# Optimization experiments

Hardware: AMD Instinct MI355X
Metric: run time of the kernel (lower is better)

The kernel has to match this reference:

```python
import jax, jax.numpy as jnp
import numpy as np

N = 100000   # nodes
E = 1600000  # edges (avg degree 16)
IN, HID, OUT = 128, 128, 64


def _glorot(key, shape):
    limit = np.sqrt(6.0 / (shape[0] + shape[1])).astype(np.float32)
    return jax.random.uniform(key, shape, jnp.float32, -limit, limit)


def setup_inputs() -> dict:
    key = jax.random.key(0)
    ks = jax.random.split(key, 12)
    inp = {}
    for i, (f, s, d) in enumerate([("feat1", "src1", "dst1"), ("feat2", "src2", "dst2"), ("feat", "src", "dst")]):
        inp[f] = jax.random.normal(ks[3 * i], (N, IN), jnp.float32)
        inp[s] = jax.random.randint(ks[3 * i + 1], (E,), 0, N, jnp.int32)
        inp[d] = jax.random.randint(ks[3 * i + 2], (E,), 0, N, jnp.int32)
    inp["W1"] = _glorot(ks[9], (IN, HID))
    inp["b1"] = jnp.zeros((HID,), jnp.float32)
    inp["W2"] = _glorot(ks[10], (HID, OUT))
    inp["b2"] = jnp.zeros((OUT,), jnp.float32)
    return inp


def _gcn_layer(x, src, dst, W, b):
    # DGL GraphConv norm='both': D_dst^{-1/2} * A * D_src^{-1/2} * X * W + b
    ones = jnp.ones(src.shape, jnp.float32)
    deg_out = jax.ops.segment_sum(ones, src, num_segments=N)
    deg_in = jax.ops.segment_sum(ones, dst, num_segments=N)
    norm_src = jax.lax.rsqrt(jnp.maximum(deg_out, 1.0))
    norm_dst = jax.lax.rsqrt(jnp.maximum(deg_in, 1.0))
    h = (x @ W) * norm_src[:, None]           # transform then normalize (math-equivalent order)
    agg = jax.ops.segment_sum(h[src], dst, num_segments=N)  # spmm aggregate
    return agg * norm_dst[:, None] + b


def _encoder(x, src, dst, W1, b1, W2, b2):
    h = jax.nn.relu(_gcn_layer(x, src, dst, W1, b1))
    return _gcn_layer(h, src, dst, W2, b2)


def reference(feat1, src1, dst1, feat2, src2, dst2, feat, src, dst, W1, b1, W2, b2):
    z1 = _encoder(feat1, src1, dst1, W1, b1, W2, b2)
    z2 = _encoder(feat2, src2, dst2, W1, b1, W2, b2)
    z = _encoder(feat, src, dst, W1, b1, W2, b2)
    return (z1, z2, z)
```

## Files before the change

kernel.cpp:

```cpp
#include <hip/hip_runtime.h>

#define NNODES 100000
#define NEDGES 1600000
#define FIN 128
#define FHID 128
#define FOUT 64

typedef unsigned short u16;
typedef unsigned char u8;
typedef unsigned int u32;
typedef __attribute__((ext_vector_type(8))) short short8;
typedef __attribute__((ext_vector_type(4))) float floatx4;

#define NBUK 391
#define NSL2 250
#define SLICE2 (NEDGES / NSL2)
#define SP ((size_t)NSL2 * NBUK)
#define NH16 ((size_t)NNODES * FHID)

__device__ __forceinline__ u16 f2bf(float f) {
  u32 u = __float_as_uint(f);
  u32 r = (u + 0x7fffu + ((u >> 16) & 1u)) >> 16;
  return (u16)r;
}

__device__ __forceinline__ const int* sel(const int* a, const int* b, const int* c, int z) {
  return z == 0 ? a : (z == 1 ? b : c);
}


__global__ __launch_bounds__(256) void bucket_hist_kernel(
    const int* s0, const int* s1, const int* s2,
    const int* d0, const int* d1, const int* d2,
    u16* __restrict__ Hbase, int E) {
  const int z = blockIdx.z;
  const int* __restrict__ src = sel(s0, s1, s2, z);
  const int* __restrict__ dst = sel(d0, d1, d2, z);
  u32* __restrict__ part = (u32*)(Hbase + (size_t)z * NH16);
  u32* __restrict__ part_src = part + SP;
  __shared__ u32 hd[NBUK], hs[NBUK];
  const int s = blockIdx.x;
  for (int i = threadIdx.x; i < NBUK; i += 256) { hd[i] = 0; hs[i] = 0; }
  __syncthreads();
  const int e0 = s * SLICE2, e1 = min(e0 + SLICE2, E);
  const int i0 = e0 >> 2, i1 = e1 >> 2;
  for (int i = i0 + threadIdx.x; i < i1; i += 256) {
    int4 dv = ((const int4*)dst)[i];
    int4 sv = ((const int4*)src)[i];
    atomicAdd(&hd[(u32)dv.x >> 8], 1u);
    atomicAdd(&hd[(u32)dv.y >> 8], 1u);
    atomicAdd(&hd[(u32)dv.z >> 8], 1u);
    atomicAdd(&hd[(u32)dv.w >> 8], 1u);
    atomicAdd(&hs[(u32)sv.x >> 8], 1u);
    atomicAdd(&hs[(u32)sv.y >> 8], 1u);
    atomicAdd(&hs[(u32)sv.z >> 8], 1u);
    atomicAdd(&hs[(u32)sv.w >> 8], 1u);
  }
  __syncthreads();
  for (int i = threadIdx.x; i < NBUK; i += 256) {
    part[(size_t)s * NBUK + i] = hd[i];
    part_src[(size_t)s * NBUK + i] = hs[i];
  }
}

__global__ __launch_bounds__(512) void scan_part_kernel(u16* __restrict__ Hbase,
                                                        u32* __restrict__ boff_d,
                                                        u32* __restrict__ bcount_d,
                                                        u32* __restrict__ boff_s,
                                                        u32* __restrict__ bcount_s) {
  const int z = blockIdx.z;
  u32* base = (u32*)(Hbase + (size_t)z * NH16);
  u32* __restrict__ part = blockIdx.x ? base + SP : base;
  u32* __restrict__ boff = (blockIdx.x ? boff_s : boff_d) + (size_t)z * NBUK;
  u32* __restrict__ bcount = (blockIdx.x ? bcount_s : bcount_d) + (size_t)z * NBUK;
  const int b = threadIdx.x;
  u32 run = 0;
  if (b < NBUK) {
#pragma unroll 5
    for (int s = 0; s < NSL2; s++) {
      u32 v = part[(size_t)s * NBUK + b];
      part[(size_t)s * NBUK + b] = run;
      run += v;
    }
  }
  __shared__ u32 sh[512];
  sh[threadIdx.x] = (b < NBUK) ? run : 0;
  __syncthreads();
  for (int d = 1; d < 512; d <<= 1) {
    u32 t = (threadIdx.x >= d) ? sh[threadIdx.x - d] : 0;
    __syncthreads();
    sh[threadIdx.x] += t;
    __syncthreads();
  }
  if (b < NBUK) {
    boff[b] = sh[threadIdx.x] - run;
    bcount[b] = run;
  }
}

__global__ __launch_bounds__(256) void scatter_kernel(
    const int* s0, const int* s1, const int* s2,
    const int* d0, const int* d1, const int* d2,
    u16* __restrict__ Hbase, u16* __restrict__ Tbase,
    const u32* __restrict__ boff_d, const u32* __restrict__ boff_src, int E) {
  const int z = blockIdx.z;
  const int* __restrict__ src = sel(s0, s1, s2, z);
  const int* __restrict__ dst = sel(d0, d1, d2, z);
  const u32* __restrict__ part = (const u32*)(Hbase + (size_t)z * NH16);
  const u32* __restrict__ part_src = part + SP;
  u8* __restrict__ pes = (u8*)(part_src + SP);
  u32* __restrict__ pe = (u32*)(Tbase + (size_t)z * NH16);
  const u32* __restrict__ boff = boff_d + (size_t)z * NBUK;
  const u32* __restrict__ boff_s = boff_src + (size_t)z * NBUK;
  __shared__ u32 cur[NBUK], curs[NBUK];
  const int s = blockIdx.x;
  for (int i = threadIdx.x; i < NBUK; i += 256) {
    cur[i] = part[(size_t)s * NBUK + i] + boff[i];
    curs[i] = part_src[(size_t)s * NBUK + i] + boff_s[i];
  }
  __syncthreads();
  const int e0 = s * SLICE2, e1 = min(e0 + SLICE2, E);
  const int i0 = e0 >> 2, i1 = e1 >> 2;
  for (int i = i0 + threadIdx.x; i < i1; i += 256) {
    int4 sv = ((const int4*)src)[i];
    int4 dv = ((const int4*)dst)[i];
    u32 p;
    p = atomicAdd(&cur[(u32)dv.x >> 8], 1u); pe[p] = ((u32)sv.x << 8) | ((u32)dv.x & 255u);
    p = atomicAdd(&cur[(u32)dv.y >> 8], 1u); pe[p] = ((u32)sv.y << 8) | ((u32)dv.y & 255u);
    p = atomicAdd(&cur[(u32)dv.z >> 8], 1u); pe[p] = ((u32)sv.z << 8) | ((u32)dv.z & 255u);
    p = atomicAdd(&cur[(u32)dv.w >> 8], 1u); pe[p] = ((u32)sv.w << 8) | ((u32)dv.w & 255u);
    p = atomicAdd(&curs[(u32)sv.x >> 8], 1u); pes[p] = (u8)((u32)sv.x & 255u);
    p = atomicAdd(&curs[(u32)sv.y >> 8], 1u); pes[p] = (u8)((u32)sv.y & 255u);
    p = atomicAdd(&curs[(u32)sv.z >> 8], 1u); pes[p] = (u8)((u32)sv.z & 255u);
    p = atomicAdd(&curs[(u32)sv.w >> 8], 1u); pes[p] = (u8)((u32)sv.w & 255u);
  }
}

__global__ __launch_bounds__(256) void bucket_finish_kernel(
    const u16* __restrict__ Tbase, const u16* __restrict__ Hbase,
    const u32* __restrict__ boffb, const u32* __restrict__ bcountb,
    const u32* __restrict__ boff_sb, const u32* __restrict__ bcount_sb,
    int* __restrict__ csrb, int* __restrict__ offsb, int* __restrict__ degb,
    float* __restrict__ ndb, float* __restrict__ nsb, int n) {
  const int z = blockIdx.z;
  const int b = blockIdx.x;
  const int t = threadIdx.x;
  if (blockIdx.y == 1) {
    const u32* partb = (const u32*)(Hbase + (size_t)z * NH16);
    const u8* __restrict__ pes = (const u8*)(partb + 2 * SP);
    const u32* boff = boff_sb + (size_t)z * NBUK;
    const u32* bcount = bcount_sb + (size_t)z * NBUK;
    float* __restrict__ norm_src = nsb + (size_t)z * NNODES;
    const int beg = (int)boff[b];
    const int cnt = (int)bcount[b];
    __shared__ int hh[256];
    hh[t] = 0;
    __syncthreads();
    for (int i = t; i < cnt; i += 256) atomicAdd(&hh[pes[beg + i]], 1);
    __syncthreads();
    const int node = b * 256 + t;
    if (node < n) norm_src[node] = rsqrtf(fmaxf((float)hh[t], 1.0f));
    return;
  }
  const u32* __restrict__ pe = (const u32*)(Tbase + (size_t)z * NH16);
  int* __restrict__ csr = csrb + (size_t)z * NEDGES;
  int* __restrict__ offs = offsb + (size_t)z * NNODES;
  int* __restrict__ deg_dst = degb + (size_t)z * NNODES;
  float* __restrict__ norm_dst = ndb + (size_t)z * NNODES;
  const u32* boff = boffb + (size_t)z * NBUK;
  const u32* bcount = bcountb + (size_t)z * NBUK;
  const int beg = (int)boff[b];
  const int cnt = (int)bcount[b];
  __shared__ int h[256], loc[256];
  h[t] = 0;
  __syncthreads();
  for (int i = t; i < cnt; i += 256) atomicAdd(&h[pe[beg + i] & 255u], 1);
  __syncthreads();
  const int myc = h[t];
  loc[t] = myc;
  __syncthreads();
  for (int d = 1; d < 256; d <<= 1) {
    int v = (t >= d) ? loc[t - d] : 0;
    __syncthreads();
    loc[t] += v;
    __syncthreads();
  }
  const int start = beg + loc[t] - myc;
  const int node = b * 256 + t;
  if (node < n) {
    offs[node] = start;
    deg_dst[node] = myc;
    norm_dst[node] = rsqrtf(fmaxf((float)myc, 1.0f));
  }
  __syncthreads();
  h[t] = start;
  __syncthreads();
  for (int i = t; i < cnt; i += 256) {
    u32 v = pe[beg + i];
    int p = atomicAdd(&h[v & 255u], 1);
    csr[p] = (int)(v >> 8);
  }
}


#define XP 136

template <int CTOT, bool IN_BF16>
__global__ __launch_bounds__(256) void gemm_mfma(const void* X0, const void* X1,
                                                 const void* X2,
                                                 const float* __restrict__ W,
                                                 const float* __restrict__ normb,
                                                 u16* __restrict__ Yb, int nrows) {
  const int z = blockIdx.z;
  const void* __restrict__ Xv = z == 0 ? X0 : (z == 1 ? X1 : X2);
  const float* __restrict__ norm = normb + (size_t)z * NNODES;
  u16* __restrict__ Y = Yb + (size_t)z * NH16;
  __shared__ u16 Xs[64 * XP];
  __shared__ u16 Wt[64 * XP];
  __shared__ float norm_s[64];
  const int tid = threadIdx.x;
  const int row0 = blockIdx.x * 64;
  const int col0 = blockIdx.y * 64;

  if constexpr (IN_BF16) {
    const u16* X = (const u16*)Xv;
    for (int i = tid; i < 64 * 16; i += 256) {
      int r = i >> 4, k8 = (i & 15) * 8;
      int gr = row0 + r;
      uint4 v = make_uint4(0u, 0u, 0u, 0u);
      if (gr < nrows) v = *(const uint4*)&X[(size_t)gr * 128 + k8];
      *(uint4*)&Xs[r * XP + k8] = v;
    }
  } else {
    const float* X = (const float*)Xv;
    for (int i = tid; i < 64 * 32; i += 256) {
      int r = i >> 5, k4 = (i & 31) * 4;
      int gr = row0 + r;
      ushort4 o = make_ushort4(0, 0, 0, 0);
      if (gr < nrows) {
        float4 v = *(const float4*)&X[(size_t)gr * 128 + k4];
        o.x = f2bf(v.x); o.y = f2bf(v.y); o.z = f2bf(v.z); o.w = f2bf(v.w);
      }
      *(ushort4*)&Xs[r * XP + k4] = o;
    }
  }
  for (int i = tid; i < 128 * 16; i += 256) {
    int k = i >> 4, c4 = (i & 15) * 4;
    float4 v = *(const float4*)&W[(size_t)k * CTOT + col0 + c4];
    Wt[(c4 + 0) * XP + k] = f2bf(v.x);
    Wt[(c4 + 1) * XP + k] = f2bf(v.y);
    Wt[(c4 + 2) * XP + k] = f2bf(v.z);
    Wt[(c4 + 3) * XP + k] = f2bf(v.w);
  }
  if (tid < 64) norm_s[tid] = (row0 + tid < nrows) ? norm[row0 + tid] : 0.f;
  __syncthreads();

  const int w = tid >> 6, lane = tid & 63;
  const int quad = lane >> 4, r16 = lane & 15;
  const int arow = w * 16 + r16;

  short8 a[4];
#pragma unroll
  for (int kc = 0; kc < 4; kc++)
    a[kc] = *(const short8*)&Xs[arow * XP + kc * 32 + quad * 8];

#pragma unroll
  for (int nc = 0; nc < 4; nc++) {
    floatx4 acc = {0.f, 0.f, 0.f, 0.f};
#pragma unroll
    for (int kc = 0; kc < 4; kc++) {
      short8 b = *(const short8*)&Wt[(nc * 16 + r16) * XP + kc * 32 + quad * 8];
      acc = __builtin_amdgcn_mfma_f32_16x16x32_bf16(a[kc], b, acc, 0, 0, 0);
    }
#pragma unroll
    for (int i = 0; i < 4; i++) {
      int lr = w * 16 + quad * 4 + i;
      int gr = row0 + lr;
      if (gr < nrows)
        Y[(size_t)gr * CTOT + col0 + nc * 16 + r16] = f2bf(acc[i] * norm_s[lr]);
    }
  }
}


__device__ __forceinline__ void acc_row(float* acc, uint4 p) {
  acc[0] += __uint_as_float(p.x << 16);
  acc[1] += __uint_as_float(p.x & 0xffff0000u);
  acc[2] += __uint_as_float(p.y << 16);
  acc[3] += __uint_as_float(p.y & 0xffff0000u);
  acc[4] += __uint_as_float(p.z << 16);
  acc[5] += __uint_as_float(p.z & 0xffff0000u);
  acc[6] += __uint_as_float(p.w << 16);
  acc[7] += __uint_as_float(p.w & 0xffff0000u);
}

template <int F>
__device__ __forceinline__ void gather_acc(const u16* __restrict__ Hp,
                                           const int* __restrict__ csr,
                                           int beg, int end, float* acc) {
  int e = beg;
  int nfull = (end - beg) >> 2;
  if (nfull > 0) {
    int sv[4]; uint4 p[4];
#pragma unroll
    for (int j = 0; j < 4; j++) sv[j] = csr[e + j];
#pragma unroll
    for (int j = 0; j < 4; j++) p[j] = *(const uint4*)&Hp[(size_t)sv[j] * F];
    for (int b = 1; b < nfull; b++) {
      e += 4;
      int s2[4]; uint4 q[4];
#pragma unroll
      for (int j = 0; j < 4; j++) s2[j] = csr[e + j];
#pragma unroll
      for (int j = 0; j < 4; j++) q[j] = *(const uint4*)&Hp[(size_t)s2[j] * F];
#pragma unroll
      for (int j = 0; j < 4; j++) acc_row(acc, p[j]);
#pragma unroll
      for (int j = 0; j < 4; j++) p[j] = q[j];
    }
#pragma unroll
    for (int j = 0; j < 4; j++) acc_row(acc, p[j]);
    e += 4;
  }
  for (; e < end; e++) {
    uint4 p = *(const uint4*)&Hp[(size_t)csr[e] * F];
    acc_row(acc, p);
  }
}


__global__ __launch_bounds__(256) void spmm1_gemm2_kernel(
    const u16* __restrict__ Hbase,
    const int* __restrict__ offsb, const int* __restrict__ degb,
    const int* __restrict__ csrb,
    const float* __restrict__ ndb, const float* __restrict__ b1,
    const float* __restrict__ W2, const float* __restrict__ nsb,
    u16* __restrict__ H2base, int n) {
  const int z = blockIdx.z;
  const u16* __restrict__ Hb = Hbase + (size_t)z * NH16;
  const int* __restrict__ offs = offsb + (size_t)z * NNODES;
  const int* __restrict__ deg = degb + (size_t)z * NNODES;
  const int* __restrict__ csr = csrb + (size_t)z * NEDGES;
  const float* __restrict__ nd = ndb + (size_t)z * NNODES;
  const float* __restrict__ ns = nsb + (size_t)z * NNODES;
  u16* __restrict__ H2 = H2base + (size_t)z * NH16;

  __shared__ u16 Ts[64 * XP];
  __shared__ u16 Wt[64 * XP];
  __shared__ float norm_s[64];
  const int tid = threadIdx.x;
  const int row0 = blockIdx.x * 64;

  for (int i = tid; i < 128 * 16; i += 256) {
    int k = i >> 4, c4 = (i & 15) * 4;
    float4 v = *(const float4*)&W2[(size_t)k * FOUT + c4];
    Wt[(c4 + 0) * XP + k] = f2bf(v.x);
    Wt[(c4 + 1) * XP + k] = f2bf(v.y);
    Wt[(c4 + 2) * XP + k] = f2bf(v.z);
    Wt[(c4 + 3) * XP + k] = f2bf(v.w);
  }
  if (tid < 64) norm_s[tid] = (row0 + tid < n) ? ns[row0 + tid] : 0.f;

  const int nsub = tid >> 4;
  const int f0 = (tid & 15) * 8;
  const u16* __restrict__ Hp = Hb + f0;
#pragma unroll
  for (int g = 0; g < 4; g++) {
    int r = g * 16 + nsub;
    int node = row0 + r;
    uint4 pk = make_uint4(0u, 0u, 0u, 0u);
    if (node < n) {
      float acc[8] = {};
      int beg = offs[node];
      gather_acc<FHID>(Hp, csr, beg, beg + deg[node], acc);
      float ndv = nd[node];
      float o[8];
#pragma unroll
      for (int i = 0; i < 8; i++)
        o[i] = fmaxf(fmaf(acc[i], ndv, b1[f0 + i]), 0.f);
      pk.x = (u32)f2bf(o[0]) | ((u32)f2bf(o[1]) << 16);
      pk.y = (u32)f2bf(o[2]) | ((u32)f2bf(o[3]) << 16);
      pk.z = (u32)f2bf(o[4]) | ((u32)f2bf(o[5]) << 16);
      pk.w = (u32)f2bf(o[6]) | ((u32)f2bf(o[7]) << 16);
    }
    *(uint4*)&Ts[r * XP + f0] = pk;
  }
  __syncthreads();

  const int w = tid >> 6, lane = tid & 63;
  const int quad = lane >> 4, r16 = lane & 15;
  const int arow = w * 16 + r16;
  short8 a[4];
#pragma unroll
  for (int kc = 0; kc < 4; kc++)
    a[kc] = *(const short8*)&Ts[arow * XP + kc * 32 + quad * 8];
#pragma unroll
  for (int nc = 0; nc < 4; nc++) {
    floatx4 acc = {0.f, 0.f, 0.f, 0.f};
#pragma unroll
    for (int kc = 0; kc < 4; kc++) {
      short8 b = *(const short8*)&Wt[(nc * 16 + r16) * XP + kc * 32 + quad * 8];
      acc = __builtin_amdgcn_mfma_f32_16x16x32_bf16(a[kc], b, acc, 0, 0, 0);
    }
#pragma unroll
    for (int i = 0; i < 4; i++) {
      int lr = w * 16 + quad * 4 + i;
      int gr = row0 + lr;
      if (gr < n)
        H2[(size_t)gr * FOUT + nc * 16 + r16] = f2bf(acc[i] * norm_s[lr]);
    }
  }
}


template <int F, bool RELU, bool OUT_BF16>
__global__ __launch_bounds__(256) void spmm_bf16(const u16* __restrict__ Hbase,
                                                 const int* __restrict__ offsb,
                                                 const int* __restrict__ degb,
                                                 const int* __restrict__ csrb,
                                                 const float* __restrict__ ndb,
                                                 const float* __restrict__ bias,
                                                 void* __restrict__ Yv, int n) {
  const int z = blockIdx.z;
  const u16* __restrict__ Hb = Hbase + (size_t)z * NH16;
  const int* __restrict__ offs = offsb + (size_t)z * NNODES;
  const int* __restrict__ deg = degb + (size_t)z * NNODES;
  const int* __restrict__ csr = csrb + (size_t)z * NEDGES;
  const float* __restrict__ norm_dst = ndb + (size_t)z * NNODES;
  constexpr int TPN = F / 8;
  constexpr int NPB = 256 / TPN;
  int node = blockIdx.x * NPB + threadIdx.x / TPN;
  if (node >= n) return;
  int f0 = (threadIdx.x % TPN) * 8;
  int beg = offs[node];
  float acc[8] = {};
  gather_acc<F>(Hb + f0, csr, beg, beg + deg[node], acc);
  float nd = norm_dst[node];
  float o[8];
#pragma unroll
  for (int i = 0; i < 8; i++) {
    o[i] = fmaf(acc[i], nd, bias[f0 + i]);
    if (RELU) o[i] = fmaxf(o[i], 0.f);
  }
  if constexpr (OUT_BF16) {
    u16* Y = (u16*)Yv + (size_t)z * NNODES * F;
    uint4 pk;
    pk.x = (u32)f2bf(o[0]) | ((u32)f2bf(o[1]) << 16);
    pk.y = (u32)f2bf(o[2]) | ((u32)f2bf(o[3]) << 16);
    pk.z = (u32)f2bf(o[4]) | ((u32)f2bf(o[5]) << 16);
    pk.w = (u32)f2bf(o[6]) | ((u32)f2bf(o[7]) << 16);
    *(uint4*)&Y[(size_t)node * F + f0] = pk;
  } else {
    float* Y = (float*)Yv + (size_t)z * NNODES * F;
    *(float4*)&Y[(size_t)node * F + f0] = make_float4(o[0], o[1], o[2], o[3]);
    *(float4*)&Y[(size_t)node * F + f0 + 4] = make_float4(o[4], o[5], o[6], o[7]);
  }
}


extern "C" void kernel_launch(void* const* d_in, const int* in_sizes, int n_in,
                              void* d_out, int out_size, void* d_ws, size_t ws_size,
                              hipStream_t stream) {
  const int N = NNODES;
  const int E = NEDGES;
  const float* W1 = (const float*)d_in[9];
  const float* b1 = (const float*)d_in[10];
  const float* W2 = (const float*)d_in[11];
  const float* b2 = (const float*)d_in[12];

  const size_t HBYTES = NH16 * 2;

  auto need_for = [&](size_t NG) -> size_t {
    size_t o = 0;
    auto al = [&](size_t b) { o = (o + b + 255) & ~(size_t)255; };
    al(NG * N * 4);
    al(NG * N * 4);
    al(NG * N * 4);
    al(NG * N * 4);
    al(NG * NBUK * 4);
    al(NG * NBUK * 4);
    al(NG * NBUK * 4);
    al(NG * NBUK * 4);
    al(NG * (size_t)E * 4);
    al(NG * HBYTES);
    al(NG * HBYTES);
    return o;
  };
  const bool batched = ws_size >= need_for(3);
  const size_t NG = batched ? 3 : 1;

  char* ws = (char*)d_ws;
  size_t off = 0;
  auto alloc = [&](size_t bytes) -> void* {
    void* p = ws + off;
    off += (bytes + 255) & ~(size_t)255;
    return p;
  };
  int* deg_dst = (int*)alloc(NG * N * 4);
  float* norm_src = (float*)alloc(NG * N * 4);
  float* norm_dst = (float*)alloc(NG * N * 4);
  int* offs = (int*)alloc(NG * N * 4);
  u32* boff = (u32*)alloc(NG * NBUK * 4);
  u32* bcount = (u32*)alloc(NG * NBUK * 4);
  u32* boff_s = (u32*)alloc(NG * NBUK * 4);
  u32* bcount_s = (u32*)alloc(NG * NBUK * 4);
  int* csr = (int*)alloc(NG * (size_t)E * 4);
  u16* H = (u16*)alloc(NG * HBYTES);
  u16* T = (u16*)alloc(NG * HBYTES);

  const int gemm_rb = (N + 63) / 64;
  const int nb2 = (N + 31) / 32;

  auto run = [&](const int* s0, const int* s1, const int* s2,
                 const int* d0, const int* d1, const int* d2,
                 const float* f0, const float* f1, const float* f2,
                 void* zoutv, unsigned gz) {
    bucket_hist_kernel<<<dim3(NSL2, 1, gz), 256, 0, stream>>>(s0, s1, s2, d0, d1, d2, H, E);
    scan_part_kernel<<<dim3(2, 1, gz), 512, 0, stream>>>(H, boff, bcount, boff_s, bcount_s);
    scatter_kernel<<<dim3(NSL2, 1, gz), 256, 0, stream>>>(s0, s1, s2, d0, d1, d2,
                                                          H, T, boff, boff_s, E);
    bucket_finish_kernel<<<dim3(NBUK, 2, gz), 256, 0, stream>>>(
        T, H, boff, bcount, boff_s, bcount_s, csr, offs, deg_dst, norm_dst,
        norm_src, N);
    gemm_mfma<FHID, false><<<dim3(gemm_rb, FHID / 64, gz), 256, 0, stream>>>(
        f0, f1, f2, W1, norm_src, H, N);
    spmm1_gemm2_kernel<<<dim3(gemm_rb, 1, gz), 256, 0, stream>>>(
        H, offs, deg_dst, csr, norm_dst, b1, W2, norm_src, T, N);
    spmm_bf16<FOUT, false, false><<<dim3(nb2, 1, gz), 256, 0, stream>>>(
        T, offs, deg_dst, csr, norm_dst, b2, zoutv, N);
  };

  if (batched) {
    run((const int*)d_in[1], (const int*)d_in[4], (const int*)d_in[7],
        (const int*)d_in[2], (const int*)d_in[5], (const int*)d_in[8],
        (const float*)d_in[0], (const float*)d_in[3], (const float*)d_in[6],
        d_out, 3);
  } else {
    for (int g = 0; g < 3; g++) {
      const float* feat = (const float*)d_in[3 * g + 0];
      const int* src = (const int*)d_in[3 * g + 1];
      const int* dst = (const int*)d_in[3 * g + 2];
      float* zout = (float*)d_out + (size_t)g * N * FOUT;
      run(src, src, src, dst, dst, dst, feat, feat, feat, zout, 1);
    }
  }
}
```

Measured before the change: 698.5 us.

## Store hidden features in 16-column chunks and split layer-one SpMM per chunk

The first GEMM now computes all 128 hidden columns per block and writes H as eight column-chunked slices (N×16 each). The fused SpMM+GEMM2 kernel is split into a per-chunk SpMM kernel, where blockIdx low bits pick the chunk so concurrent blocks gather from a smaller working set that fits in cache. A separate GEMM2 then reads the chunked layout. CSR index loads in that SpMM become nontemporal. The cost is reading the CSR eight times, plus one extra kernel launch and an intermediate round trip through memory.

```diff
diff --git a/kernel.cpp b/kernel.cpp
--- a/kernel.cpp
+++ b/kernel.cpp
@@ -17,6 +17,9 @@
 #define SLICE2 (NEDGES / NSL2)
 #define SP ((size_t)NSL2 * NBUK)
 #define NH16 ((size_t)NNODES * FHID)
+#define NCHUNK 8
+#define CSL ((size_t)NNODES * 16)
+#define NGRP 782
 
 __device__ __forceinline__ u16 f2bf(float f) {
   u32 u = __float_as_uint(f);
@@ -202,51 +205,37 @@
   }
 }
 
-
 #define XP 136
 
-template <int CTOT, bool IN_BF16>
-__global__ __launch_bounds__(256) void gemm_mfma(const void* X0, const void* X1,
-                                                 const void* X2,
-                                                 const float* __restrict__ W,
-                                                 const float* __restrict__ normb,
-                                                 u16* __restrict__ Yb, int nrows) {
-  const int z = blockIdx.z;
-  const void* __restrict__ Xv = z == 0 ? X0 : (z == 1 ? X1 : X2);
+
+__global__ __launch_bounds__(256) void gemm1_kernel(const float* X0, const float* X1,
+                                                    const float* X2,
+                                                    const float* __restrict__ W,
+                                                    const float* __restrict__ normb,
+                                                    u16* __restrict__ Yb, int nrows) {
+  const int z = blockIdx.z;
+  const float* __restrict__ X = z == 0 ? (const float*)X0 : (z == 1 ? (const float*)X1 : (const float*)X2);
   const float* __restrict__ norm = normb + (size_t)z * NNODES;
-  u16* __restrict__ Y = Yb + (size_t)z * NH16;
+  u16* __restrict__ Y8 = Yb + (size_t)z * NH16;
   __shared__ u16 Xs[64 * XP];
-  __shared__ u16 Wt[64 * XP];
+  __shared__ u16 Wt[128 * XP];
   __shared__ float norm_s[64];
   const int tid = threadIdx.x;
   const int row0 = blockIdx.x * 64;
-  const int col0 = blockIdx.y * 64;
-
-  if constexpr (IN_BF16) {
-    const u16* X = (const u16*)Xv;
-    for (int i = tid; i < 64 * 16; i += 256) {
-      int r = i >> 4, k8 = (i & 15) * 8;
-      int gr = row0 + r;
-      uint4 v = make_uint4(0u, 0u, 0u, 0u);
-      if (gr < nrows) v = *(const uint4*)&X[(size_t)gr * 128 + k8];
-      *(uint4*)&Xs[r * XP + k8] = v;
-    }
-  } else {
-    const float* X = (const float*)Xv;
-    for (int i = tid; i < 64 * 32; i += 256) {
-      int r = i >> 5, k4 = (i & 31) * 4;
-      int gr = row0 + r;
-      ushort4 o = make_ushort4(0, 0, 0, 0);
-      if (gr < nrows) {
-        float4 v = *(const float4*)&X[(size_t)gr * 128 + k4];
-        o.x = f2bf(v.x); o.y = f2bf(v.y); o.z = f2bf(v.z); o.w = f2bf(v.w);
-      }
-      *(ushort4*)&Xs[r * XP + k4] = o;
-    }
-  }
-  for (int i = tid; i < 128 * 16; i += 256) {
-    int k = i >> 4, c4 = (i & 15) * 4;
-    float4 v = *(const float4*)&W[(size_t)k * CTOT + col0 + c4];
+
+  for (int i = tid; i < 64 * 32; i += 256) {
+    int r = i >> 5, k4 = (i & 31) * 4;
+    int gr = row0 + r;
+    ushort4 o = make_ushort4(0, 0, 0, 0);
+    if (gr < nrows) {
+      float4 v = *(const float4*)&X[(size_t)gr * 128 + k4];
+      o.x = f2bf(v.x); o.y = f2bf(v.y); o.z = f2bf(v.z); o.w = f2bf(v.w);
+    }
+    *(ushort4*)&Xs[r * XP + k4] = o;
+  }
+  for (int i = tid; i < 128 * 32; i += 256) {
+    int k = i >> 5, c4 = (i & 31) * 4;
+    float4 v = *(const float4*)&W[(size_t)k * FHID + c4];
     Wt[(c4 + 0) * XP + k] = f2bf(v.x);
     Wt[(c4 + 1) * XP + k] = f2bf(v.y);
     Wt[(c4 + 2) * XP + k] = f2bf(v.z);
@@ -265,7 +254,7 @@
     a[kc] = *(const short8*)&Xs[arow * XP + kc * 32 + quad * 8];
 
 #pragma unroll
-  for (int nc = 0; nc < 4; nc++) {
+  for (int nc = 0; nc < 8; nc++) {
     floatx4 acc = {0.f, 0.f, 0.f, 0.f};
 #pragma unroll
     for (int kc = 0; kc < 4; kc++) {
@@ -277,7 +266,7 @@
       int lr = w * 16 + quad * 4 + i;
       int gr = row0 + lr;
       if (gr < nrows)
-        Y[(size_t)gr * CTOT + col0 + nc * 16 + r16] = f2bf(acc[i] * norm_s[lr]);
+        Y8[(size_t)nc * CSL + (size_t)gr * 16 + r16] = f2bf(acc[i] * norm_s[lr]);
     }
   }
 }
@@ -294,23 +283,27 @@
   acc[7] += __uint_as_float(p.w & 0xffff0000u);
 }
 
-template <int F>
+template <int F, bool NT>
 __device__ __forceinline__ void gather_acc(const u16* __restrict__ Hp,
                                            const int* __restrict__ csr,
                                            int beg, int end, float* acc) {
+  auto ldc = [&](int e) -> int {
+    if constexpr (NT) return __builtin_nontemporal_load(&csr[e]);
+    else return csr[e];
+  };
   int e = beg;
   int nfull = (end - beg) >> 2;
   if (nfull > 0) {
     int sv[4]; uint4 p[4];
 #pragma unroll
-    for (int j = 0; j < 4; j++) sv[j] = csr[e + j];
+    for (int j = 0; j < 4; j++) sv[j] = ldc(e + j);
 #pragma unroll
     for (int j = 0; j < 4; j++) p[j] = *(const uint4*)&Hp[(size_t)sv[j] * F];
     for (int b = 1; b < nfull; b++) {
       e += 4;
       int s2[4]; uint4 q[4];
 #pragma unroll
-      for (int j = 0; j < 4; j++) s2[j] = csr[e + j];
+      for (int j = 0; j < 4; j++) s2[j] = ldc(e + j);
 #pragma unroll
       for (int j = 0; j < 4; j++) q[j] = *(const uint4*)&Hp[(size_t)s2[j] * F];
 #pragma unroll
@@ -323,77 +316,91 @@
     e += 4;
   }
   for (; e < end; e++) {
-    uint4 p = *(const uint4*)&Hp[(size_t)csr[e] * F];
+    uint4 p = *(const uint4*)&Hp[(size_t)ldc(e) * F];
     acc_row(acc, p);
   }
 }
 
 
-__global__ __launch_bounds__(256) void spmm1_gemm2_kernel(
-    const u16* __restrict__ Hbase,
+__global__ __launch_bounds__(256) void spmm1_chunk_kernel(
+    const u16* __restrict__ H8base,
     const int* __restrict__ offsb, const int* __restrict__ degb,
     const int* __restrict__ csrb,
     const float* __restrict__ ndb, const float* __restrict__ b1,
-    const float* __restrict__ W2, const float* __restrict__ nsb,
-    u16* __restrict__ H2base, int n) {
-  const int z = blockIdx.z;
-  const u16* __restrict__ Hb = Hbase + (size_t)z * NH16;
+    u16* __restrict__ T8base, int n) {
+  const int z = blockIdx.z;
+  const int c = blockIdx.x & 7;
+  const int grp = blockIdx.x >> 3;
+  const u16* __restrict__ Hc = H8base + (size_t)z * NH16 + (size_t)c * CSL;
+  u16* __restrict__ Tc = T8base + (size_t)z * NH16 + (size_t)c * CSL;
   const int* __restrict__ offs = offsb + (size_t)z * NNODES;
   const int* __restrict__ deg = degb + (size_t)z * NNODES;
   const int* __restrict__ csr = csrb + (size_t)z * NEDGES;
   const float* __restrict__ nd = ndb + (size_t)z * NNODES;
-  const float* __restrict__ ns = nsb + (size_t)z * NNODES;
-  u16* __restrict__ H2 = H2base + (size_t)z * NH16;
-
-  __shared__ u16 Ts[64 * XP];
+
+  const int node = grp * 128 + (threadIdx.x >> 1);
+  if (node >= n) return;
+  const int half = threadIdx.x & 1;
+  const int f0 = c * 16 + half * 8;
+  int beg = offs[node];
+  float acc[8] = {};
+  gather_acc<16, true>(Hc + half * 8, csr, beg, beg + deg[node], acc);
+  float ndv = nd[node];
+  float o[8];
+#pragma unroll
+  for (int i = 0; i < 8; i++)
+    o[i] = fmaxf(fmaf(acc[i], ndv, b1[f0 + i]), 0.f);
+  uint4 pk;
+  pk.x = (u32)f2bf(o[0]) | ((u32)f2bf(o[1]) << 16);
+  pk.y = (u32)f2bf(o[2]) | ((u32)f2bf(o[3]) << 16);
+  pk.z = (u32)f2bf(o[4]) | ((u32)f2bf(o[5]) << 16);
+  pk.w = (u32)f2bf(o[6]) | ((u32)f2bf(o[7]) << 16);
+  *(uint4*)&Tc[(size_t)node * 16 + half * 8] = pk;
+}
+
+
+__global__ __launch_bounds__(256) void gemm2_kernel(const u16* __restrict__ T8base,
+                                                    const float* __restrict__ W,
+                                                    const float* __restrict__ normb,
+                                                    u16* __restrict__ Yb, int nrows) {
+  const int z = blockIdx.z;
+  const u16* __restrict__ X8 = T8base + (size_t)z * NH16;
+  const float* __restrict__ norm = normb + (size_t)z * NNODES;
+  u16* __restrict__ Y = Yb + (size_t)z * NH16;
+  __shared__ u16 Xs[64 * XP];
   __shared__ u16 Wt[64 * XP];
   __shared__ float norm_s[64];
   const int tid = threadIdx.x;
   const int row0 = blockIdx.x * 64;
 
+  for (int i = tid; i < 64 * 16; i += 256) {
+    int r = i >> 4, k8 = (i & 15) * 8;
+    int gr = row0 + r;
+    uint4 v = make_uint4(0u, 0u, 0u, 0u);
+    if (gr < nrows)
+      v = *(const uint4*)&X8[(size_t)(k8 >> 4) * CSL + (size_t)gr * 16 + (k8 & 15)];
+    *(uint4*)&Xs[r * XP + k8] = v;
+  }
   for (int i = tid; i < 128 * 16; i += 256) {
     int k = i >> 4, c4 = (i & 15) * 4;
-    float4 v = *(const float4*)&W2[(size_t)k * FOUT + c4];
+    float4 v = *(const float4*)&W[(size_t)k * FOUT + c4];
     Wt[(c4 + 0) * XP + k] = f2bf(v.x);
     Wt[(c4 + 1) * XP + k] = f2bf(v.y);
     Wt[(c4 + 2) * XP + k] = f2bf(v.z);
     Wt[(c4 + 3) * XP + k] = f2bf(v.w);
   }
-  if (tid < 64) norm_s[tid] = (row0 + tid < n) ? ns[row0 + tid] : 0.f;
-
-  const int nsub = tid >> 4;
-  const int f0 = (tid & 15) * 8;
-  const u16* __restrict__ Hp = Hb + f0;
-#pragma unroll
-  for (int g = 0; g < 4; g++) {
-    int r = g * 16 + nsub;
-    int node = row0 + r;
-    uint4 pk = make_uint4(0u, 0u, 0u, 0u);
-    if (node < n) {
-      float acc[8] = {};
-      int beg = offs[node];
-      gather_acc<FHID>(Hp, csr, beg, beg + deg[node], acc);
-      float ndv = nd[node];
-      float o[8];
-#pragma unroll
-      for (int i = 0; i < 8; i++)
-        o[i] = fmaxf(fmaf(acc[i], ndv, b1[f0 + i]), 0.f);
-      pk.x = (u32)f2bf(o[0]) | ((u32)f2bf(o[1]) << 16);
-      pk.y = (u32)f2bf(o[2]) | ((u32)f2bf(o[3]) << 16);
-      pk.z = (u32)f2bf(o[4]) | ((u32)f2bf(o[5]) << 16);
-      pk.w = (u32)f2bf(o[6]) | ((u32)f2bf(o[7]) << 16);
-    }
-    *(uint4*)&Ts[r * XP + f0] = pk;
-  }
+  if (tid < 64) norm_s[tid] = (row0 + tid < nrows) ? norm[row0 + tid] : 0.f;
   __syncthreads();
 
   const int w = tid >> 6, lane = tid & 63;
   const int quad = lane >> 4, r16 = lane & 15;
   const int arow = w * 16 + r16;
+
   short8 a[4];
 #pragma unroll
   for (int kc = 0; kc < 4; kc++)
-    a[kc] = *(const short8*)&Ts[arow * XP + kc * 32 + quad * 8];
+    a[kc] = *(const short8*)&Xs[arow * XP + kc * 32 + quad * 8];
+
 #pragma unroll
   for (int nc = 0; nc < 4; nc++) {
     floatx4 acc = {0.f, 0.f, 0.f, 0.f};
@@ -406,8 +413,8 @@
     for (int i = 0; i < 4; i++) {
       int lr = w * 16 + quad * 4 + i;
       int gr = row0 + lr;
-      if (gr < n)
-        H2[(size_t)gr * FOUT + nc * 16 + r16] = f2bf(acc[i] * norm_s[lr]);
+      if (gr < nrows)
+        Y[(size_t)gr * FOUT + nc * 16 + r16] = f2bf(acc[i] * norm_s[lr]);
     }
   }
 }
@@ -434,7 +441,7 @@
   int f0 = (threadIdx.x % TPN) * 8;
   int beg = offs[node];
   float acc[8] = {};
-  gather_acc<F>(Hb + f0, csr, beg, beg + deg[node], acc);
+  gather_acc<F, false>(Hb + f0, csr, beg, beg + deg[node], acc);
   float nd = norm_dst[node];
   float o[8];
 #pragma unroll
@@ -510,6 +517,7 @@
 
   const int gemm_rb = (N + 63) / 64;
   const int nb2 = (N + 31) / 32;
+  const int spmm1_gx = NCHUNK * NGRP;
 
   auto run = [&](const int* s0, const int* s1, const int* s2,
                  const int* d0, const int* d1, const int* d2,
@@ -522,12 +530,14 @@
     bucket_finish_kernel<<<dim3(NBUK, 2, gz), 256, 0, stream>>>(
         T, H, boff, bcount, boff_s, bcount_s, csr, offs, deg_dst, norm_dst,
         norm_src, N);
-    gemm_mfma<FHID, false><<<dim3(gemm_rb, FHID / 64, gz), 256, 0, stream>>>(
+    gemm1_kernel<<<dim3(gemm_rb, 1, gz), 256, 0, stream>>>(
         f0, f1, f2, W1, norm_src, H, N);
-    spmm1_gemm2_kernel<<<dim3(gemm_rb, 1, gz), 256, 0, stream>>>(
-        H, offs, deg_dst, csr, norm_dst, b1, W2, norm_src, T, N);
+    spmm1_chunk_kernel<<<dim3(spmm1_gx, 1, gz), 256, 0, stream>>>(
+        H, offs, deg_dst, csr, norm_dst, b1, T, N);
+    gemm2_kernel<<<dim3(gemm_rb, 1, gz), 256, 0, stream>>>(
+        T, W2, norm_src, H, N);
     spmm_bf16<FOUT, false, false><<<dim3(nb2, 1, gz), 256, 0, stream>>>(
-        T, offs, deg_dst, csr, norm_dst, b2, zoutv, N);
+        H, offs, deg_dst, csr, norm_dst, b2, zoutv, N);
   };
 
   if (batched) {
```

Result: slower. 944.2 us (+35.2%).
